# Optimization experiments

Hardware: AMD Instinct MI355X
Metric: run time of the kernel (lower is better)

The kernel has to match this reference:

```python
import jax, jax.numpy as jnp
import numpy as np
from jax import lax

B = 32768
IMG = 28
K = 3
OUT_HW = IMG - K + 1  # 26
FLAT = OUT_HW * OUT_HW  # 676
HID = 300
NCLS = 10


def setup_inputs() -> dict:
    key = jax.random.key(0)
    ks = jax.random.split(key, 8)
    x = jax.random.normal(ks[0], (B, IMG * IMG), dtype=jnp.float32)
    conv_w = jax.random.normal(ks[1], (K, K), dtype=jnp.float32) * 0.1
    # Linear params stored as (in, out) so forward is h @ W + b
    W1 = jax.random.normal(ks[2], (FLAT, HID), dtype=jnp.float32) * 0.04
    b1 = jnp.zeros((HID,), dtype=jnp.float32)
    W2 = jax.random.normal(ks[3], (HID, HID), dtype=jnp.float32) * 0.06
    b2 = jnp.zeros((HID,), dtype=jnp.float32)
    W3 = jax.random.normal(ks[4], (HID, NCLS), dtype=jnp.float32) * 0.06
    b3 = jnp.zeros((NCLS,), dtype=jnp.float32)
    return {"x": x, "conv_w": conv_w, "W1": W1, "b1": b1,
            "W2": W2, "b2": b2, "W3": W3, "b3": b3}


def reference(x, conv_w, W1, b1, W2, b2, W3, b3):
    b = x.shape[0]
    img = x.reshape(b, 1, IMG, IMG)  # NCHW
    # Valid cross-correlation with 3x3 kernel -> [B,1,26,26]
    y = lax.conv_general_dilated(
        img, conv_w[None, None, :, :], window_strides=(1, 1), padding="VALID",
        dimension_numbers=("NCHW", "OIHW", "NCHW"))
    h = y.reshape(b, FLAT)
    h = jax.nn.relu(h @ W1 + b1)
    h = jax.nn.relu(h @ W2 + b2)
    return h @ W3 + b3
```

## Files before the change

### kernel.cpp

```cpp
#include <hip/hip_runtime.h>


typedef __bf16 bf16_t;
typedef __bf16 bf16x4 __attribute__((ext_vector_type(4)));
typedef __bf16 bf16x8 __attribute__((ext_vector_type(8)));
typedef float  f32x4  __attribute__((ext_vector_type(4)));

#define MFMA16(a, b, c) __builtin_amdgcn_mfma_f32_16x16x32_bf16((a), (b), (c), 0, 0, 0)

#define W1F_ELEMS (25 * 20 * 64 * 8)
#define W2F_ELEMS (10 * 20 * 64 * 8)
#define W3F_ELEMS (10 * 1 * 64 * 8)
#define ASTRIDE   136

__global__ void prep_weights(const float* __restrict__ conv_w,
                             const float* __restrict__ W1,
                             const float* __restrict__ W2,
                             const float* __restrict__ W3,
                             bf16_t* __restrict__ W1f,
                             bf16_t* __restrict__ W2f,
                             bf16_t* __restrict__ W3f) {
    int idx = blockIdx.x * 256 + threadIdx.x;
    if (idx < 800 * 320) {
        int k = idx / 320;
        int n = idx - k * 320;
        float v = 0.0f;
        if (k < 784 && n < 300) {
            int py = k / 28;
            int px = k - py * 28;
#pragma unroll
            for (int ky = 0; ky < 3; ++ky) {
                int oy = py - ky;
                if (oy < 0 || oy > 25) continue;
#pragma unroll
                for (int kx = 0; kx < 3; ++kx) {
                    int ox = px - kx;
                    if (ox < 0 || ox > 25) continue;
                    v += conv_w[ky * 3 + kx] * W1[(oy * 26 + ox) * 300 + n];
                }
            }
        }
        int kc = k >> 5, quad = (k >> 3) & 3, j = k & 7;
        int nt = n >> 4, nin = n & 15;
        W1f[(((kc * 20 + nt) * 64 + quad * 16 + nin) << 3) + j] = (bf16_t)v;
    } else if (idx < 800 * 320 + 320 * 320) {
        int i2 = idx - 800 * 320;
        int k = i2 / 320;
        int n = i2 - k * 320;
        float v = (k < 300 && n < 300) ? W2[k * 300 + n] : 0.0f;
        int kc = k >> 5, quad = (k >> 3) & 3, j = k & 7;
        int nt = n >> 4, nin = n & 15;
        W2f[(((kc * 20 + nt) * 64 + quad * 16 + nin) << 3) + j] = (bf16_t)v;
    } else if (idx < 800 * 320 + 320 * 320 + 320 * 16) {
        int i3 = idx - (800 * 320 + 320 * 320);
        int k = i3 / 16;
        int n = i3 - k * 16;
        float v = (k < 300 && n < 10) ? W3[k * 10 + n] : 0.0f;
        int kc = k >> 5, quad = (k >> 3) & 3, j = k & 7;
        W3f[(((kc * 64) + quad * 16 + n) << 3) + j] = (bf16_t)v;
    }
}

__device__ __forceinline__ void stage16(const bf16x8* g, bf16x8* l) {
    __builtin_amdgcn_global_load_lds(
        (const __attribute__((address_space(1))) void*)g,
        (__attribute__((address_space(3))) void*)l, 16, 0, 0);
}

__global__ __launch_bounds__(512, 4) void fused_mlp(
    const float* __restrict__ x, const float* __restrict__ b1,
    const float* __restrict__ b2, const float* __restrict__ b3,
    const bf16x8* __restrict__ W1f, const bf16x8* __restrict__ W2f,
    const bf16x8* __restrict__ W3f, float* __restrict__ out) {
    __shared__ bf16x8 bufB1[2 * 1280];
    __shared__ bf16_t Abuf[64 * ASTRIDE];
    __shared__ bf16x8 bufB2[1280];

    bf16x8* hbuf = bufB1;

    const int tid = threadIdx.x;
    const int w   = tid >> 6;
    const int l   = tid & 63;
    const int mh  = w & 1;
    const int nq  = w >> 1;
    const int q   = l >> 4;
    const int l15 = l & 15;
    const int r0  = blockIdx.x * 64;

    const int srow = tid >> 5;
    const int sc4  = tid & 31;
    const int trow = tid >> 3;
    const int tc4  = tid & 7;

    for (int t = w; t < 20; t += 8) stage16(W1f + (t * 64 + l), bufB1 + t * 64);
    for (int t = w; t < 20; t += 8) stage16(W2f + (t * 64 + l), bufB2 + t * 64);

    float4 pf[4];
#pragma unroll
    for (int i = 0; i < 4; ++i)
        pf[i] = *(const float4*)(x + (size_t)(r0 + i * 16 + srow) * 784 + sc4 * 4);

    f32x4 acc[2][5];
#pragma unroll
    for (int m = 0; m < 2; ++m)
#pragma unroll
        for (int nt = 0; nt < 5; ++nt) acc[m][nt] = (f32x4){0.f, 0.f, 0.f, 0.f};

    int kc = 0;
    for (int band = 0; band < 7; ++band) {
        __syncthreads();

        if (band < 6) {
#pragma unroll
            for (int i = 0; i < 4; ++i) {
                bf16x4 v;
                v[0] = (bf16_t)pf[i].x; v[1] = (bf16_t)pf[i].y;
                v[2] = (bf16_t)pf[i].z; v[3] = (bf16_t)pf[i].w;
                *(bf16x4*)&Abuf[(i * 16 + srow) * ASTRIDE + sc4 * 4] = v;
            }
        } else {
            bf16x4 v;
            v[0] = (bf16_t)pf[0].x; v[1] = (bf16_t)pf[0].y;
            v[2] = (bf16_t)pf[0].z; v[3] = (bf16_t)pf[0].w;
            *(bf16x4*)&Abuf[trow * ASTRIDE + tc4 * 4] = v;
        }

        if (band + 1 < 6) {
#pragma unroll
            for (int i = 0; i < 4; ++i)
                pf[i] = *(const float4*)(x + (size_t)(r0 + i * 16 + srow) * 784 +
                                         (band + 1) * 128 + sc4 * 4);
        } else if (band + 1 == 6) {
            pf[0] = (tc4 < 4)
                ? *(const float4*)(x + (size_t)(r0 + trow) * 784 + 768 + tc4 * 4)
                : make_float4(0.f, 0.f, 0.f, 0.f);
        }

        const int nch = (band < 6) ? 4 : 1;
        for (int kcl = 0; kcl < nch; ++kcl, ++kc) {
            __syncthreads();

            if (kc + 1 < 25) {
                int s1 = (kc + 1) & 1;
                for (int t = w; t < 20; t += 8)
                    stage16(W1f + (((kc + 1) * 20 + t) * 64 + l),
                            bufB1 + s1 * 1280 + t * 64);
            }

            bf16x8 afA = *(const bf16x8*)&Abuf[(mh * 32 + l15) * ASTRIDE +
                                               kcl * 32 + q * 8];
            bf16x8 afB = *(const bf16x8*)&Abuf[(mh * 32 + 16 + l15) * ASTRIDE +
                                               kcl * 32 + q * 8];
            const bf16x8* bb = bufB1 + (kc & 1) * 1280 + (nq * 5) * 64 + l;
#pragma unroll
            for (int nt = 0; nt < 5; ++nt) {
                bf16x8 b = bb[nt * 64];
                acc[0][nt] = MFMA16(afA, b, acc[0][nt]);
                acc[1][nt] = MFMA16(afB, b, acc[1][nt]);
            }
        }
    }
    __syncthreads();

    {
        bf16_t* hb = (bf16_t*)hbuf;
#pragma unroll
        for (int nt = 0; nt < 5; ++nt) {
            int n = (nq * 5 + nt) * 16 + l15;
            float bias = (n < 300) ? b1[n] : 0.0f;
            int kc2 = n >> 5, quad = (n >> 3) & 3, j = n & 7;
#pragma unroll
            for (int mt2 = 0; mt2 < 2; ++mt2) {
                int mt = mh * 2 + mt2;
#pragma unroll
                for (int r = 0; r < 4; ++r) {
                    float v = acc[mt2][nt][r] + bias;
                    v = v > 0.f ? v : 0.f;
                    hb[(((kc2 * 4 + mt) * 64 + quad * 16 + q * 4 + r) << 3) + j] =
                        (bf16_t)v;
                }
            }
        }
    }
    __syncthreads();

#pragma unroll
    for (int m = 0; m < 2; ++m)
#pragma unroll
        for (int nt = 0; nt < 5; ++nt) acc[m][nt] = (f32x4){0.f, 0.f, 0.f, 0.f};
    for (int kc2 = 0; kc2 < 10; ++kc2) {
        bf16x8 a0 = hbuf[(kc2 * 4 + mh * 2 + 0) * 64 + l];
        bf16x8 a1 = hbuf[(kc2 * 4 + mh * 2 + 1) * 64 + l];
        const bf16x8* bb = bufB2 + (nq * 5) * 64 + l;
#pragma unroll
        for (int nt = 0; nt < 5; ++nt) {
            bf16x8 b = bb[nt * 64];
            acc[0][nt] = MFMA16(a0, b, acc[0][nt]);
            acc[1][nt] = MFMA16(a1, b, acc[1][nt]);
        }
        if (kc2 + 1 < 10) {
            __syncthreads();
            for (int t = w; t < 20; t += 8)
                stage16(W2f + (((kc2 + 1) * 20 + t) * 64 + l), bufB2 + t * 64);
            __syncthreads();
        }
    }
    __syncthreads();

    {
        bf16_t* hb = (bf16_t*)hbuf;
#pragma unroll
        for (int nt = 0; nt < 5; ++nt) {
            int n = (nq * 5 + nt) * 16 + l15;
            float bias = (n < 300) ? b2[n] : 0.0f;
            int kc2 = n >> 5, quad = (n >> 3) & 3, j = n & 7;
#pragma unroll
            for (int mt2 = 0; mt2 < 2; ++mt2) {
                int mt = mh * 2 + mt2;
#pragma unroll
                for (int r = 0; r < 4; ++r) {
                    float v = acc[mt2][nt][r] + bias;
                    v = v > 0.f ? v : 0.f;
                    hb[(((kc2 * 4 + mt) * 64 + quad * 16 + q * 4 + r) << 3) + j] =
                        (bf16_t)v;
                }
            }
        }
    }
    __syncthreads();

    if (w < 4) {
        f32x4 acc3 = (f32x4){0.f, 0.f, 0.f, 0.f};
#pragma unroll
        for (int kc3 = 0; kc3 < 10; ++kc3)
            acc3 = MFMA16(hbuf[(kc3 * 4 + w) * 64 + l], W3f[kc3 * 64 + l], acc3);
        if (l15 < 10) {
            float bias = b3[l15];
#pragma unroll
            for (int r = 0; r < 4; ++r)
                out[(size_t)(r0 + w * 16 + q * 4 + r) * 10 + l15] = acc3[r] + bias;
        }
    }
}

extern "C" void kernel_launch(void* const* d_in, const int* in_sizes, int n_in,
                              void* d_out, int out_size, void* d_ws, size_t ws_size,
                              hipStream_t stream) {
    const float* x      = (const float*)d_in[0];
    const float* conv_w = (const float*)d_in[1];
    const float* W1     = (const float*)d_in[2];
    const float* b1     = (const float*)d_in[3];
    const float* W2     = (const float*)d_in[4];
    const float* b2     = (const float*)d_in[5];
    const float* W3     = (const float*)d_in[6];
    const float* b3     = (const float*)d_in[7];
    float* out = (float*)d_out;

    char* ws = (char*)d_ws;
    bf16_t* W1f = (bf16_t*)(ws);
    bf16_t* W2f = (bf16_t*)(ws + (size_t)W1F_ELEMS * 2);
    bf16_t* W3f = (bf16_t*)(ws + (size_t)(W1F_ELEMS + W2F_ELEMS) * 2);
    if (ws_size < (size_t)(W1F_ELEMS + W2F_ELEMS + W3F_ELEMS) * 2) return;

    int prep_total = 800 * 320 + 320 * 320 + 320 * 16;
    prep_weights<<<(prep_total + 255) / 256, 256, 0, stream>>>(
        conv_w, W1, W2, W3, W1f, W2f, W3f);

    fused_mlp<<<32768 / 64, 512, 0, stream>>>(
        x, b1, b2, b3, (const bf16x8*)W1f, (const bf16x8*)W2f,
        (const bf16x8*)W3f, out);
}
```

Before: 190.1 us.

## Read weights directly from global memory and retile warps over full M

New measurement: 197.4 us. +3.8%, slower.

```diff
diff --git a/kernel.cpp b/kernel.cpp
--- a/kernel.cpp
+++ b/kernel.cpp
@@ -13,58 +13,68 @@
 #define W3F_ELEMS (10 * 1 * 64 * 8)
 #define ASTRIDE   136
 
-__global__ void prep_weights(const float* __restrict__ conv_w,
-                             const float* __restrict__ W1,
-                             const float* __restrict__ W2,
-                             const float* __restrict__ W3,
-                             bf16_t* __restrict__ W1f,
-                             bf16_t* __restrict__ W2f,
-                             bf16_t* __restrict__ W3f) {
+#define W1F_GRP 32000
+#define W2F_GRP 12800
+#define W3F_GRP 640
+
+__global__ __launch_bounds__(256) void prep_weights(
+    const float* __restrict__ conv_w, const float* __restrict__ W1,
+    const float* __restrict__ W2, const float* __restrict__ W3,
+    bf16x8* __restrict__ W1f, bf16x8* __restrict__ W2f,
+    bf16x8* __restrict__ W3f) {
     int idx = blockIdx.x * 256 + threadIdx.x;
-    if (idx < 800 * 320) {
-        int k = idx / 320;
-        int n = idx - k * 320;
-        float v = 0.0f;
-        if (k < 784 && n < 300) {
-            int py = k / 28;
-            int px = k - py * 28;
-#pragma unroll
-            for (int ky = 0; ky < 3; ++ky) {
-                int oy = py - ky;
-                if (oy < 0 || oy > 25) continue;
-#pragma unroll
-                for (int kx = 0; kx < 3; ++kx) {
-                    int ox = px - kx;
-                    if (ox < 0 || ox > 25) continue;
-                    v += conv_w[ky * 3 + kx] * W1[(oy * 26 + ox) * 300 + n];
+    if (idx < W1F_GRP) {
+        int within = idx & 63, quad = within >> 4, nin = within & 15;
+        int t = idx >> 6;
+        int nt = t % 20, kcv = t / 20;
+        int kb = kcv * 32 + quad * 8, n = nt * 16 + nin;
+        bf16x8 vec;
+#pragma unroll
+        for (int j = 0; j < 8; ++j) {
+            int k = kb + j;
+            float v = 0.0f;
+            if (k < 784 && n < 300) {
+                int py = k / 28, px = k - py * 28;
+#pragma unroll
+                for (int ky = 0; ky < 3; ++ky) {
+                    int oy = py - ky;
+                    if (oy < 0 || oy > 25) continue;
+#pragma unroll
+                    for (int kx = 0; kx < 3; ++kx) {
+                        int ox = px - kx;
+                        if (ox < 0 || ox > 25) continue;
+                        v += conv_w[ky * 3 + kx] * W1[(oy * 26 + ox) * 300 + n];
+                    }
                 }
             }
-        }
-        int kc = k >> 5, quad = (k >> 3) & 3, j = k & 7;
-        int nt = n >> 4, nin = n & 15;
-        W1f[(((kc * 20 + nt) * 64 + quad * 16 + nin) << 3) + j] = (bf16_t)v;
-    } else if (idx < 800 * 320 + 320 * 320) {
-        int i2 = idx - 800 * 320;
-        int k = i2 / 320;
-        int n = i2 - k * 320;
-        float v = (k < 300 && n < 300) ? W2[k * 300 + n] : 0.0f;
-        int kc = k >> 5, quad = (k >> 3) & 3, j = k & 7;
-        int nt = n >> 4, nin = n & 15;
-        W2f[(((kc * 20 + nt) * 64 + quad * 16 + nin) << 3) + j] = (bf16_t)v;
-    } else if (idx < 800 * 320 + 320 * 320 + 320 * 16) {
-        int i3 = idx - (800 * 320 + 320 * 320);
-        int k = i3 / 16;
-        int n = i3 - k * 16;
-        float v = (k < 300 && n < 10) ? W3[k * 10 + n] : 0.0f;
-        int kc = k >> 5, quad = (k >> 3) & 3, j = k & 7;
-        W3f[(((kc * 64) + quad * 16 + n) << 3) + j] = (bf16_t)v;
-    }
-}
-
-__device__ __forceinline__ void stage16(const bf16x8* g, bf16x8* l) {
-    __builtin_amdgcn_global_load_lds(
-        (const __attribute__((address_space(1))) void*)g,
-        (__attribute__((address_space(3))) void*)l, 16, 0, 0);
+            vec[j] = (bf16_t)v;
+        }
+        W1f[idx] = vec;
+    } else if (idx < W1F_GRP + W2F_GRP) {
+        int g = idx - W1F_GRP;
+        int within = g & 63, quad = within >> 4, nin = within & 15;
+        int t = g >> 6;
+        int nt = t % 20, kcv = t / 20;
+        int kb = kcv * 32 + quad * 8, n = nt * 16 + nin;
+        bf16x8 vec;
+#pragma unroll
+        for (int j = 0; j < 8; ++j) {
+            int k = kb + j;
+            vec[j] = (bf16_t)((k < 300 && n < 300) ? W2[k * 300 + n] : 0.0f);
+        }
+        W2f[g] = vec;
+    } else if (idx < W1F_GRP + W2F_GRP + W3F_GRP) {
+        int g = idx - (W1F_GRP + W2F_GRP);
+        int within = g & 63, quad = within >> 4, n = within & 15;
+        int kcv = g >> 6, kb = kcv * 32 + quad * 8;
+        bf16x8 vec;
+#pragma unroll
+        for (int j = 0; j < 8; ++j) {
+            int k = kb + j;
+            vec[j] = (bf16_t)((k < 300 && n < 10) ? W3[k * 10 + n] : 0.0f);
+        }
+        W3f[g] = vec;
+    }
 }
 
 __global__ __launch_bounds__(512, 4) void fused_mlp(
@@ -72,39 +82,37 @@
     const float* __restrict__ b2, const float* __restrict__ b3,
     const bf16x8* __restrict__ W1f, const bf16x8* __restrict__ W2f,
     const bf16x8* __restrict__ W3f, float* __restrict__ out) {
-    __shared__ bf16x8 bufB1[2 * 1280];
     __shared__ bf16_t Abuf[64 * ASTRIDE];
-    __shared__ bf16x8 bufB2[1280];
-
-    bf16x8* hbuf = bufB1;
+    __shared__ bf16x8 hbuf[40 * 64];
 
     const int tid = threadIdx.x;
     const int w   = tid >> 6;
     const int l   = tid & 63;
-    const int mh  = w & 1;
-    const int nq  = w >> 1;
     const int q   = l >> 4;
     const int l15 = l & 15;
     const int r0  = blockIdx.x * 64;
+
+    const bool t3   = (w < 4);
+    const int  nt0  = t3 ? (w * 3) : (12 + (w - 4) * 2);
+    const int  boff2 = t3 ? 128 : 64;
 
     const int srow = tid >> 5;
     const int sc4  = tid & 31;
     const int trow = tid >> 3;
     const int tc4  = tid & 7;
 
-    for (int t = w; t < 20; t += 8) stage16(W1f + (t * 64 + l), bufB1 + t * 64);
-    for (int t = w; t < 20; t += 8) stage16(W2f + (t * 64 + l), bufB2 + t * 64);
-
     float4 pf[4];
 #pragma unroll
     for (int i = 0; i < 4; ++i)
         pf[i] = *(const float4*)(x + (size_t)(r0 + i * 16 + srow) * 784 + sc4 * 4);
 
-    f32x4 acc[2][5];
-#pragma unroll
-    for (int m = 0; m < 2; ++m)
-#pragma unroll
-        for (int nt = 0; nt < 5; ++nt) acc[m][nt] = (f32x4){0.f, 0.f, 0.f, 0.f};
+    f32x4 acc[4][3];
+#pragma unroll
+    for (int m = 0; m < 4; ++m)
+#pragma unroll
+        for (int j = 0; j < 3; ++j) acc[m][j] = (f32x4){0.f, 0.f, 0.f, 0.f};
+
+    const bf16x8* bB1 = W1f + nt0 * 64 + l;
 
     int kc = 0;
     for (int band = 0; band < 7; ++band) {
@@ -136,97 +144,100 @@
                 : make_float4(0.f, 0.f, 0.f, 0.f);
         }
 
-        const int nch = (band < 6) ? 4 : 1;
-        for (int kcl = 0; kcl < nch; ++kcl, ++kc) {
-            __syncthreads();
-
-            if (kc + 1 < 25) {
-                int s1 = (kc + 1) & 1;
-                for (int t = w; t < 20; t += 8)
-                    stage16(W1f + (((kc + 1) * 20 + t) * 64 + l),
-                            bufB1 + s1 * 1280 + t * 64);
-            }
-
-            bf16x8 afA = *(const bf16x8*)&Abuf[(mh * 32 + l15) * ASTRIDE +
-                                               kcl * 32 + q * 8];
-            bf16x8 afB = *(const bf16x8*)&Abuf[(mh * 32 + 16 + l15) * ASTRIDE +
-                                               kcl * 32 + q * 8];
-            const bf16x8* bb = bufB1 + (kc & 1) * 1280 + (nq * 5) * 64 + l;
-#pragma unroll
-            for (int nt = 0; nt < 5; ++nt) {
-                bf16x8 b = bb[nt * 64];
-                acc[0][nt] = MFMA16(afA, b, acc[0][nt]);
-                acc[1][nt] = MFMA16(afB, b, acc[1][nt]);
-            }
-        }
-    }
+        __syncthreads();
+
+#define G1CHUNK(KCL)                                                            \
+        {                                                                       \
+            bf16x8 a0 = *(const bf16x8*)&Abuf[( 0 + l15) * ASTRIDE + (KCL) * 32 + q * 8]; \
+            bf16x8 a1 = *(const bf16x8*)&Abuf[(16 + l15) * ASTRIDE + (KCL) * 32 + q * 8]; \
+            bf16x8 a2 = *(const bf16x8*)&Abuf[(32 + l15) * ASTRIDE + (KCL) * 32 + q * 8]; \
+            bf16x8 a3 = *(const bf16x8*)&Abuf[(48 + l15) * ASTRIDE + (KCL) * 32 + q * 8]; \
+            const bf16x8* bp = bB1 + kc * 1280;                                 \
+            bf16x8 b0 = bp[0], b1v = bp[64], b2v = bp[boff2];                   \
+            acc[0][0] = MFMA16(a0, b0, acc[0][0]);                              \
+            acc[1][0] = MFMA16(a1, b0, acc[1][0]);                              \
+            acc[2][0] = MFMA16(a2, b0, acc[2][0]);                              \
+            acc[3][0] = MFMA16(a3, b0, acc[3][0]);                              \
+            acc[0][1] = MFMA16(a0, b1v, acc[0][1]);                             \
+            acc[1][1] = MFMA16(a1, b1v, acc[1][1]);                             \
+            acc[2][1] = MFMA16(a2, b1v, acc[2][1]);                             \
+            acc[3][1] = MFMA16(a3, b1v, acc[3][1]);                             \
+            if (t3) {                                                           \
+                acc[0][2] = MFMA16(a0, b2v, acc[0][2]);                         \
+                acc[1][2] = MFMA16(a1, b2v, acc[1][2]);                         \
+                acc[2][2] = MFMA16(a2, b2v, acc[2][2]);                         \
+                acc[3][2] = MFMA16(a3, b2v, acc[3][2]);                         \
+            }                                                                   \
+            ++kc;                                                               \
+        }
+
+        if (band < 6) {
+            G1CHUNK(0) G1CHUNK(1) G1CHUNK(2) G1CHUNK(3)
+        } else {
+            G1CHUNK(0)
+        }
+    }
+
+    bf16_t* hb = (bf16_t*)hbuf;
+
+#define HSTORE(J, BIAS)                                                         \
+    {                                                                           \
+        int n = (nt0 + (J)) * 16 + l15;                                         \
+        float bias = (n < 300) ? (BIAS)[n] : 0.0f;                              \
+        int kh = n >> 5, quad = (n >> 3) & 3, jj = n & 7;                       \
+        for (int mt = 0; mt < 4; ++mt)                                          \
+            for (int r = 0; r < 4; ++r) {                                       \
+                float v = acc[mt][(J)][r] + bias;                               \
+                v = v > 0.f ? v : 0.f;                                          \
+                hb[(((kh * 4 + mt) * 64 + quad * 16 + q * 4 + r) << 3) + jj] =  \
+                    (bf16_t)v;                                                  \
+            }                                                                   \
+    }
+
+    HSTORE(0, b1)
+    HSTORE(1, b1)
+    if (t3) HSTORE(2, b1)
     __syncthreads();
 
-    {
-        bf16_t* hb = (bf16_t*)hbuf;
-#pragma unroll
-        for (int nt = 0; nt < 5; ++nt) {
-            int n = (nq * 5 + nt) * 16 + l15;
-            float bias = (n < 300) ? b1[n] : 0.0f;
-            int kc2 = n >> 5, quad = (n >> 3) & 3, j = n & 7;
-#pragma unroll
-            for (int mt2 = 0; mt2 < 2; ++mt2) {
-                int mt = mh * 2 + mt2;
-#pragma unroll
-                for (int r = 0; r < 4; ++r) {
-                    float v = acc[mt2][nt][r] + bias;
-                    v = v > 0.f ? v : 0.f;
-                    hb[(((kc2 * 4 + mt) * 64 + quad * 16 + q * 4 + r) << 3) + j] =
-                        (bf16_t)v;
-                }
-            }
-        }
-    }
+#pragma unroll
+    for (int m = 0; m < 4; ++m)
+#pragma unroll
+        for (int j = 0; j < 3; ++j) acc[m][j] = (f32x4){0.f, 0.f, 0.f, 0.f};
+
+    const bf16x8* bB2 = W2f + nt0 * 64 + l;
+
+#define G2CHUNK(KC2)                                                            \
+    {                                                                           \
+        bf16x8 a0 = hbuf[((KC2) * 4 + 0) * 64 + l];                             \
+        bf16x8 a1 = hbuf[((KC2) * 4 + 1) * 64 + l];                             \
+        bf16x8 a2 = hbuf[((KC2) * 4 + 2) * 64 + l];                             \
+        bf16x8 a3 = hbuf[((KC2) * 4 + 3) * 64 + l];                             \
+        const bf16x8* bp = bB2 + (KC2) * 1280;                                  \
+        bf16x8 b0 = bp[0], b1v = bp[64], b2v = bp[boff2];                       \
+        acc[0][0] = MFMA16(a0, b0, acc[0][0]);                                  \
+        acc[1][0] = MFMA16(a1, b0, acc[1][0]);                                  \
+        acc[2][0] = MFMA16(a2, b0, acc[2][0]);                                  \
+        acc[3][0] = MFMA16(a3, b0, acc[3][0]);                                  \
+        acc[0][1] = MFMA16(a0, b1v, acc[0][1]);                                 \
+        acc[1][1] = MFMA16(a1, b1v, acc[1][1]);                                 \
+        acc[2][1] = MFMA16(a2, b1v, acc[2][1]);                                 \
+        acc[3][1] = MFMA16(a3, b1v, acc[3][1]);                                 \
+        if (t3) {                                                               \
+            acc[0][2] = MFMA16(a0, b2v, acc[0][2]);                             \
+            acc[1][2] = MFMA16(a1, b2v, acc[1][2]);                             \
+            acc[2][2] = MFMA16(a2, b2v, acc[2][2]);                             \
+            acc[3][2] = MFMA16(a3, b2v, acc[3][2]);                             \
+        }                                                                       \
+    }
+
+    G2CHUNK(0) G2CHUNK(1) G2CHUNK(2) G2CHUNK(3) G2CHUNK(4)
+    G2CHUNK(5) G2CHUNK(6) G2CHUNK(7) G2CHUNK(8) G2CHUNK(9)
+
     __syncthreads();
 
-#pragma unroll
-    for (int m = 0; m < 2; ++m)
-#pragma unroll
-        for (int nt = 0; nt < 5; ++nt) acc[m][nt] = (f32x4){0.f, 0.f, 0.f, 0.f};
-    for (int kc2 = 0; kc2 < 10; ++kc2) {
-        bf16x8 a0 = hbuf[(kc2 * 4 + mh * 2 + 0) * 64 + l];
-        bf16x8 a1 = hbuf[(kc2 * 4 + mh * 2 + 1) * 64 + l];
-        const bf16x8* bb = bufB2 + (nq * 5) * 64 + l;
-#pragma unroll
-        for (int nt = 0; nt < 5; ++nt) {
-            bf16x8 b = bb[nt * 64];
-            acc[0][nt] = MFMA16(a0, b, acc[0][nt]);
-            acc[1][nt] = MFMA16(a1, b, acc[1][nt]);
-        }
-        if (kc2 + 1 < 10) {
-            __syncthreads();
-            for (int t = w; t < 20; t += 8)
-                stage16(W2f + (((kc2 + 1) * 20 + t) * 64 + l), bufB2 + t * 64);
-            __syncthreads();
-        }
-    }
-    __syncthreads();
-
-    {
-        bf16_t* hb = (bf16_t*)hbuf;
-#pragma unroll
-        for (int nt = 0; nt < 5; ++nt) {
-            int n = (nq * 5 + nt) * 16 + l15;
-            float bias = (n < 300) ? b2[n] : 0.0f;
-            int kc2 = n >> 5, quad = (n >> 3) & 3, j = n & 7;
-#pragma unroll
-            for (int mt2 = 0; mt2 < 2; ++mt2) {
-                int mt = mh * 2 + mt2;
-#pragma unroll
-                for (int r = 0; r < 4; ++r) {
-                    float v = acc[mt2][nt][r] + bias;
-                    v = v > 0.f ? v : 0.f;
-                    hb[(((kc2 * 4 + mt) * 64 + quad * 16 + q * 4 + r) << 3) + j] =
-                        (bf16_t)v;
-                }
-            }
-        }
-    }
+    HSTORE(0, b2)
+    HSTORE(1, b2)
+    if (t3) HSTORE(2, b2)
     __syncthreads();
 
     if (w < 4) {
@@ -262,9 +273,9 @@
     bf16_t* W3f = (bf16_t*)(ws + (size_t)(W1F_ELEMS + W2F_ELEMS) * 2);
     if (ws_size < (size_t)(W1F_ELEMS + W2F_ELEMS + W3F_ELEMS) * 2) return;
 
-    int prep_total = 800 * 320 + 320 * 320 + 320 * 16;
+    int prep_total = W1F_GRP + W2F_GRP + W3F_GRP;
     prep_weights<<<(prep_total + 255) / 256, 256, 0, stream>>>(
-        conv_w, W1, W2, W3, W1f, W2f, W3f);
+        conv_w, W1, W2, W3, (bf16x8*)W1f, (bf16x8*)W2f, (bf16x8*)W3f);
 
     fused_mlp<<<32768 / 64, 512, 0, stream>>>(
         x, b1, b2, b3, (const bf16x8*)W1f, (const bf16x8*)W2f,
```

## Stream fp32 x via direct-to-LDS triple buffer, read weights from global, reassign N tiles

Applied to the files above, without the earlier changes.

New measurement: 191.9 us. Within noise of the previous version (+0.9%).

```diff
diff --git a/kernel.cpp b/kernel.cpp
--- a/kernel.cpp
+++ b/kernel.cpp
@@ -2,7 +2,6 @@
 
 
 typedef __bf16 bf16_t;
-typedef __bf16 bf16x4 __attribute__((ext_vector_type(4)));
 typedef __bf16 bf16x8 __attribute__((ext_vector_type(8)));
 typedef float  f32x4  __attribute__((ext_vector_type(4)));
 
@@ -11,7 +10,8 @@
 #define W1F_ELEMS (25 * 20 * 64 * 8)
 #define W2F_ELEMS (10 * 20 * 64 * 8)
 #define W3F_ELEMS (10 * 1 * 64 * 8)
-#define ASTRIDE   136
+
+#define SLOT_BYTES 16384
 
 __global__ void prep_weights(const float* __restrict__ conv_w,
                              const float* __restrict__ W1,
@@ -61,7 +61,7 @@
     }
 }
 
-__device__ __forceinline__ void stage16(const bf16x8* g, bf16x8* l) {
+__device__ __forceinline__ void stage16(const void* g, void* l) {
     __builtin_amdgcn_global_load_lds(
         (const __attribute__((address_space(1))) void*)g,
         (__attribute__((address_space(3))) void*)l, 16, 0, 0);
@@ -72,162 +72,199 @@
     const float* __restrict__ b2, const float* __restrict__ b3,
     const bf16x8* __restrict__ W1f, const bf16x8* __restrict__ W2f,
     const bf16x8* __restrict__ W3f, float* __restrict__ out) {
-    __shared__ bf16x8 bufB1[2 * 1280];
-    __shared__ bf16_t Abuf[64 * ASTRIDE];
-    __shared__ bf16x8 bufB2[1280];
-
-    bf16x8* hbuf = bufB1;
+    __shared__ __align__(16) unsigned char smem[3 * SLOT_BYTES];
+    bf16x8* hbuf = (bf16x8*)smem;
+    bf16_t* hb   = (bf16_t*)smem;
 
     const int tid = threadIdx.x;
     const int w   = tid >> 6;
     const int l   = tid & 63;
-    const int mh  = w & 1;
-    const int nq  = w >> 1;
     const int q   = l >> 4;
     const int l15 = l & 15;
     const int r0  = blockIdx.x * 64;
 
-    const int srow = tid >> 5;
-    const int sc4  = tid & 31;
-    const int trow = tid >> 3;
-    const int tc4  = tid & 7;
-
-    for (int t = w; t < 20; t += 8) stage16(W1f + (t * 64 + l), bufB1 + t * 64);
-    for (int t = w; t < 20; t += 8) stage16(W2f + (t * 64 + l), bufB2 + t * 64);
-
-    float4 pf[4];
-#pragma unroll
-    for (int i = 0; i < 4; ++i)
-        pf[i] = *(const float4*)(x + (size_t)(r0 + i * 16 + srow) * 784 + sc4 * 4);
-
-    f32x4 acc[2][5];
-#pragma unroll
-    for (int m = 0; m < 2; ++m)
-#pragma unroll
-        for (int nt = 0; nt < 5; ++nt) acc[m][nt] = (f32x4){0.f, 0.f, 0.f, 0.f};
-
-    int kc = 0;
-    for (int band = 0; band < 7; ++band) {
-        __syncthreads();
-
-        if (band < 6) {
-#pragma unroll
-            for (int i = 0; i < 4; ++i) {
-                bf16x4 v;
-                v[0] = (bf16_t)pf[i].x; v[1] = (bf16_t)pf[i].y;
-                v[2] = (bf16_t)pf[i].z; v[3] = (bf16_t)pf[i].w;
-                *(bf16x4*)&Abuf[(i * 16 + srow) * ASTRIDE + sc4 * 4] = v;
-            }
-        } else {
-            bf16x4 v;
-            v[0] = (bf16_t)pf[0].x; v[1] = (bf16_t)pf[0].y;
-            v[2] = (bf16_t)pf[0].z; v[3] = (bf16_t)pf[0].w;
-            *(bf16x4*)&Abuf[trow * ASTRIDE + tc4 * 4] = v;
-        }
-
-        if (band + 1 < 6) {
-#pragma unroll
-            for (int i = 0; i < 4; ++i)
-                pf[i] = *(const float4*)(x + (size_t)(r0 + i * 16 + srow) * 784 +
-                                         (band + 1) * 128 + sc4 * 4);
-        } else if (band + 1 == 6) {
-            pf[0] = (tc4 < 4)
-                ? *(const float4*)(x + (size_t)(r0 + trow) * 784 + 768 + tc4 * 4)
-                : make_float4(0.f, 0.f, 0.f, 0.f);
-        }
-
-        const int nch = (band < 6) ? 4 : 1;
-        for (int kcl = 0; kcl < nch; ++kcl, ++kc) {
-            __syncthreads();
-
-            if (kc + 1 < 25) {
-                int s1 = (kc + 1) & 1;
-                for (int t = w; t < 20; t += 8)
-                    stage16(W1f + (((kc + 1) * 20 + t) * 64 + l),
-                            bufB1 + s1 * 1280 + t * 64);
-            }
-
-            bf16x8 afA = *(const bf16x8*)&Abuf[(mh * 32 + l15) * ASTRIDE +
-                                               kcl * 32 + q * 8];
-            bf16x8 afB = *(const bf16x8*)&Abuf[(mh * 32 + 16 + l15) * ASTRIDE +
-                                               kcl * 32 + q * 8];
-            const bf16x8* bb = bufB1 + (kc & 1) * 1280 + (nq * 5) * 64 + l;
-#pragma unroll
-            for (int nt = 0; nt < 5; ++nt) {
-                bf16x8 b = bb[nt * 64];
-                acc[0][nt] = MFMA16(afA, b, acc[0][nt]);
-                acc[1][nt] = MFMA16(afB, b, acc[1][nt]);
-            }
-        }
-    }
-    __syncthreads();
-
+    const bool t3    = (w < 4);
+    const int  nt0   = t3 ? (w * 3) : (12 + (w - 4) * 2);
+    const int  boff2 = t3 ? 128 : 64;
+
+    f32x4 acc[4][3];
+#pragma unroll
+    for (int m = 0; m < 4; ++m)
+#pragma unroll
+        for (int j = 0; j < 3; ++j) acc[m][j] = (f32x4){0.f, 0.f, 0.f, 0.f};
+
+    const bf16x8* bB1 = W1f + nt0 * 64 + l;
+
+#define STAGE_BAND(BAND)                                                       \
+    {                                                                          \
+        unsigned char* slot_ = smem + ((BAND) % 3) * SLOT_BYTES;               \
+        if ((BAND) < 12) {                                                     \
+            _Pragma("unroll")                                                  \
+            for (int i_ = 0; i_ < 2; ++i_) {                                   \
+                int row_ = w * 8 + i_ * 4 + (l >> 4);                          \
+                int u_   = (l & 15) ^ (row_ & 7);                              \
+                stage16(x + (size_t)(r0 + row_) * 784 + (BAND) * 64 + u_ * 4,  \
+                        slot_ + w * 2048 + i_ * 1024);                         \
+            }                                                                  \
+        } else {                                                               \
+            int row_ = w * 8 + (l >> 3);                                       \
+            int u_   = (l & 7) ^ (row_ & 7);                                   \
+            const float* src_ = x + (size_t)(r0 + row_) * 784 +                \
+                                ((u_ < 4) ? (768 + u_ * 4) : 0);               \
+            stage16(src_, slot_ + w * 1024);                                   \
+        }                                                                      \
+    }
+
+#define AFRAG(DST, SLOT, RS, KCL, MT)                                          \
+    {                                                                          \
+        int row_ = (MT) * 16 + l15;                                            \
+        int r7_  = row_ & 7;                                                   \
+        float4 fa_ = *(const float4*)((SLOT) + row_ * (RS) +                   \
+                     ((((KCL) * 8 + q * 2 + 0) ^ r7_) << 4));                  \
+        float4 fb_ = *(const float4*)((SLOT) + row_ * (RS) +                   \
+                     ((((KCL) * 8 + q * 2 + 1) ^ r7_) << 4));                  \
+        bf16x8 t_;                                                             \
+        t_[0] = (bf16_t)fa_.x; t_[1] = (bf16_t)fa_.y;                          \
+        t_[2] = (bf16_t)fa_.z; t_[3] = (bf16_t)fa_.w;                          \
+        t_[4] = (bf16_t)fb_.x; t_[5] = (bf16_t)fb_.y;                          \
+        t_[6] = (bf16_t)fb_.z; t_[7] = (bf16_t)fb_.w;                          \
+        DST = t_;                                                              \
+    }
+
+#define G1CHUNK(SLOT, RS, KCL, KC)                                             \
+    {                                                                          \
+        bf16x8 a0, a1, a2, a3;                                                 \
+        AFRAG(a0, SLOT, RS, KCL, 0) AFRAG(a1, SLOT, RS, KCL, 1)                \
+        AFRAG(a2, SLOT, RS, KCL, 2) AFRAG(a3, SLOT, RS, KCL, 3)                \
+        const bf16x8* bp = bB1 + (KC) * 1280;                                  \
+        bf16x8 b0 = bp[0], b1v = bp[64], b2v = bp[boff2];                      \
+        acc[0][0] = MFMA16(a0, b0, acc[0][0]);                                 \
+        acc[1][0] = MFMA16(a1, b0, acc[1][0]);                                 \
+        acc[2][0] = MFMA16(a2, b0, acc[2][0]);                                 \
+        acc[3][0] = MFMA16(a3, b0, acc[3][0]);                                 \
+        acc[0][1] = MFMA16(a0, b1v, acc[0][1]);                                \
+        acc[1][1] = MFMA16(a1, b1v, acc[1][1]);                                \
+        acc[2][1] = MFMA16(a2, b1v, acc[2][1]);                                \
+        acc[3][1] = MFMA16(a3, b1v, acc[3][1]);                                \
+        if (t3) {                                                              \
+            acc[0][2] = MFMA16(a0, b2v, acc[0][2]);                            \
+            acc[1][2] = MFMA16(a1, b2v, acc[1][2]);                            \
+            acc[2][2] = MFMA16(a2, b2v, acc[2][2]);                            \
+            acc[3][2] = MFMA16(a3, b2v, acc[3][2]);                            \
+        }                                                                      \
+    }
+
+#define VMW(N) asm volatile("s_waitcnt vmcnt(" #N ") lgkmcnt(0)" ::: "memory")
+#define BARRIER()                         \
+    __builtin_amdgcn_s_barrier();         \
+    __builtin_amdgcn_sched_barrier(0)
+
+    STAGE_BAND(0)
+    STAGE_BAND(1)
+
+    VMW(2);
+    BARRIER();
+    STAGE_BAND(2)
+    __builtin_amdgcn_sched_barrier(0);
     {
-        bf16_t* hb = (bf16_t*)hbuf;
-#pragma unroll
-        for (int nt = 0; nt < 5; ++nt) {
-            int n = (nq * 5 + nt) * 16 + l15;
-            float bias = (n < 300) ? b1[n] : 0.0f;
-            int kc2 = n >> 5, quad = (n >> 3) & 3, j = n & 7;
-#pragma unroll
-            for (int mt2 = 0; mt2 < 2; ++mt2) {
-                int mt = mh * 2 + mt2;
-#pragma unroll
-                for (int r = 0; r < 4; ++r) {
-                    float v = acc[mt2][nt][r] + bias;
-                    v = v > 0.f ? v : 0.f;
-                    hb[(((kc2 * 4 + mt) * 64 + quad * 16 + q * 4 + r) << 3) + j] =
-                        (bf16_t)v;
-                }
-            }
-        }
-    }
-    __syncthreads();
-
-#pragma unroll
-    for (int m = 0; m < 2; ++m)
-#pragma unroll
-        for (int nt = 0; nt < 5; ++nt) acc[m][nt] = (f32x4){0.f, 0.f, 0.f, 0.f};
-    for (int kc2 = 0; kc2 < 10; ++kc2) {
-        bf16x8 a0 = hbuf[(kc2 * 4 + mh * 2 + 0) * 64 + l];
-        bf16x8 a1 = hbuf[(kc2 * 4 + mh * 2 + 1) * 64 + l];
-        const bf16x8* bb = bufB2 + (nq * 5) * 64 + l;
-#pragma unroll
-        for (int nt = 0; nt < 5; ++nt) {
-            bf16x8 b = bb[nt * 64];
-            acc[0][nt] = MFMA16(a0, b, acc[0][nt]);
-            acc[1][nt] = MFMA16(a1, b, acc[1][nt]);
-        }
-        if (kc2 + 1 < 10) {
-            __syncthreads();
-            for (int t = w; t < 20; t += 8)
-                stage16(W2f + (((kc2 + 1) * 20 + t) * 64 + l), bufB2 + t * 64);
-            __syncthreads();
-        }
-    }
-    __syncthreads();
-
+        unsigned char* s0 = smem;
+        G1CHUNK(s0, 256, 0, 0)
+        G1CHUNK(s0, 256, 1, 1)
+    }
+
+    for (int band = 1; band <= 10; ++band) {
+        if (t3) { VMW(8); } else { VMW(6); }
+        BARRIER();
+        STAGE_BAND(band + 2)
+        __builtin_amdgcn_sched_barrier(0);
+        unsigned char* sb = smem + (band % 3) * SLOT_BYTES;
+        int kc = band * 2;
+        G1CHUNK(sb, 256, 0, kc)
+        G1CHUNK(sb, 256, 1, kc + 1)
+    }
+
+    if (t3) { VMW(7); } else { VMW(5); }
+    BARRIER();
     {
-        bf16_t* hb = (bf16_t*)hbuf;
-#pragma unroll
-        for (int nt = 0; nt < 5; ++nt) {
-            int n = (nq * 5 + nt) * 16 + l15;
-            float bias = (n < 300) ? b2[n] : 0.0f;
-            int kc2 = n >> 5, quad = (n >> 3) & 3, j = n & 7;
-#pragma unroll
-            for (int mt2 = 0; mt2 < 2; ++mt2) {
-                int mt = mh * 2 + mt2;
-#pragma unroll
-                for (int r = 0; r < 4; ++r) {
-                    float v = acc[mt2][nt][r] + bias;
-                    v = v > 0.f ? v : 0.f;
-                    hb[(((kc2 * 4 + mt) * 64 + quad * 16 + q * 4 + r) << 3) + j] =
-                        (bf16_t)v;
-                }
-            }
-        }
-    }
-    __syncthreads();
+        unsigned char* sb = smem + (11 % 3) * SLOT_BYTES;
+        G1CHUNK(sb, 256, 0, 22)
+        G1CHUNK(sb, 256, 1, 23)
+    }
+
+    if (t3) { VMW(6); } else { VMW(4); }
+    BARRIER();
+    {
+        unsigned char* sb = smem + (12 % 3) * SLOT_BYTES;
+        G1CHUNK(sb, 128, 0, 24)
+    }
+
+    asm volatile("s_waitcnt lgkmcnt(0)" ::: "memory");
+    BARRIER();
+
+#define HSTORE(J, BIAS)                                                        \
+    {                                                                          \
+        int n = (nt0 + (J)) * 16 + l15;                                        \
+        float bias = (n < 300) ? (BIAS)[n] : 0.0f;                             \
+        int kh = n >> 5, quad = (n >> 3) & 3, jj = n & 7;                      \
+        _Pragma("unroll")                                                      \
+        for (int mt = 0; mt < 4; ++mt)                                         \
+            _Pragma("unroll")                                                  \
+            for (int r = 0; r < 4; ++r) {                                      \
+                float v = acc[mt][(J)][r] + bias;                              \
+                v = v > 0.f ? v : 0.f;                                         \
+                hb[(((kh * 4 + mt) * 64 + quad * 16 + q * 4 + r) << 3) + jj] = \
+                    (bf16_t)v;                                                 \
+            }                                                                  \
+    }
+
+    HSTORE(0, b1)
+    HSTORE(1, b1)
+    if (t3) HSTORE(2, b1)
+    asm volatile("s_waitcnt lgkmcnt(0)" ::: "memory");
+    BARRIER();
+
+#pragma unroll
+    for (int m = 0; m < 4; ++m)
+#pragma unroll
+        for (int j = 0; j < 3; ++j) acc[m][j] = (f32x4){0.f, 0.f, 0.f, 0.f};
+
+    const bf16x8* bB2 = W2f + nt0 * 64 + l;
+
+#define G2CHUNK(KC2)                                                           \
+    {                                                                          \
+        bf16x8 a0 = hbuf[((KC2) * 4 + 0) * 64 + l];                            \
+        bf16x8 a1 = hbuf[((KC2) * 4 + 1) * 64 + l];                            \
+        bf16x8 a2 = hbuf[((KC2) * 4 + 2) * 64 + l];                            \
+        bf16x8 a3 = hbuf[((KC2) * 4 + 3) * 64 + l];                            \
+        const bf16x8* bp = bB2 + (KC2) * 1280;                                 \
+        bf16x8 b0 = bp[0], b1v = bp[64], b2v = bp[boff2];                      \
+        acc[0][0] = MFMA16(a0, b0, acc[0][0]);                                 \
+        acc[1][0] = MFMA16(a1, b0, acc[1][0]);                                 \
+        acc[2][0] = MFMA16(a2, b0, acc[2][0]);                                 \
+        acc[3][0] = MFMA16(a3, b0, acc[3][0]);                                 \
+        acc[0][1] = MFMA16(a0, b1v, acc[0][1]);                                \
+        acc[1][1] = MFMA16(a1, b1v, acc[1][1]);                                \
+        acc[2][1] = MFMA16(a2, b1v, acc[2][1]);                                \
+        acc[3][1] = MFMA16(a3, b1v, acc[3][1]);                                \
+        if (t3) {                                                              \
+            acc[0][2] = MFMA16(a0, b2v, acc[0][2]);                            \
+            acc[1][2] = MFMA16(a1, b2v, acc[1][2]);                            \
+            acc[2][2] = MFMA16(a2, b2v, acc[2][2]);                            \
+            acc[3][2] = MFMA16(a3, b2v, acc[3][2]);                            \
+        }                                                                      \
+    }
+
+    G2CHUNK(0) G2CHUNK(1) G2CHUNK(2) G2CHUNK(3) G2CHUNK(4)
+    G2CHUNK(5) G2CHUNK(6) G2CHUNK(7) G2CHUNK(8) G2CHUNK(9)
+
+    asm volatile("s_waitcnt lgkmcnt(0)" ::: "memory");
+    BARRIER();
+
+    HSTORE(0, b2)
+    HSTORE(1, b2)
+    if (t3) HSTORE(2, b2)
+    asm volatile("s_waitcnt lgkmcnt(0)" ::: "memory");
+    BARRIER();
 
     if (w < 4) {
         f32x4 acc3 = (f32x4){0.f, 0.f, 0.f, 0.f};
```
